# Kernel tuning notes

Measured on AMD Instinct MI355X. Metric: run time of the kernel, lower is better.

The kernel has to match this reference:

```python
import jax, jax.numpy as jnp
import numpy as np

B, C, CI, H, W = 4, 128, 64, 96, 96  # batch, in_channels, inter_channels, spatial
SS = 2                                # sub_sample_factor (maxpool on phi and g)
BN_EPS = 1e-5


def conv1x1(x, w, b):
    # x: [B,C,H,W], w: [O,C], b: [O]
    return jnp.einsum('bchw,oc->bohw', x, w) + b[None, :, None, None]


def maxpool2(x):
    # 2x2 max pool, stride 2. x: [B,C,H,W]
    b, c, h, w = x.shape
    return x.reshape(b, c, h // 2, 2, w // 2, 2).max(axis=(3, 5))


def setup_inputs() -> dict:
    key = jax.random.key(0)
    ks = jax.random.split(key, 12)
    s_in = 1.0 / np.sqrt(C)
    s_ci = 1.0 / np.sqrt(CI)
    return {
        'x':        jax.random.normal(ks[0], (B, C, H, W), jnp.float32),
        'g_w':      jax.random.normal(ks[1], (CI, C), jnp.float32) * s_in,
        'g_b':      jax.random.normal(ks[2], (CI,), jnp.float32) * 0.01,
        'theta_w':  jax.random.normal(ks[3], (CI, C), jnp.float32) * s_in,
        'theta_b':  jax.random.normal(ks[4], (CI,), jnp.float32) * 0.01,
        'phi_w':    jax.random.normal(ks[5], (CI, C), jnp.float32) * s_in,
        'phi_b':    jax.random.normal(ks[6], (CI,), jnp.float32) * 0.01,
        'W_w':      jax.random.normal(ks[7], (C, CI), jnp.float32) * s_ci,
        'W_b':      jax.random.normal(ks[8], (C,), jnp.float32) * 0.01,
        'bn_gamma': jax.random.normal(ks[9], (C,), jnp.float32) * 0.1 + 1.0,
        'bn_beta':  jax.random.normal(ks[10], (C,), jnp.float32) * 0.1,
        'bn_mean':  jax.random.normal(ks[11], (C,), jnp.float32) * 0.1,
        'bn_var':   jax.random.uniform(jax.random.fold_in(key, 99), (C,), jnp.float32, 0.5, 1.5),
    }


def reference(x, g_w, g_b, theta_w, theta_b, phi_w, phi_b, W_w, W_b,
              bn_gamma, bn_beta, bn_mean, bn_var):
    b = x.shape[0]
    # g: conv1x1 -> maxpool(2) -> [B, N_kv, CI]
    g_x = maxpool2(conv1x1(x, g_w, g_b)).reshape(b, CI, -1).transpose(0, 2, 1)
    # theta: conv1x1 -> [B, N_q, CI]
    theta_x = conv1x1(x, theta_w, theta_b).reshape(b, CI, -1).transpose(0, 2, 1)
    # phi: conv1x1 -> maxpool(2) -> [B, CI, N_kv]
    phi_x = maxpool2(conv1x1(x, phi_w, phi_b)).reshape(b, CI, -1)
    # full affinity [B, N_q, N_kv], softmax over keys (embedded_gaussian)
    f = jnp.einsum('bqc,bck->bqk', theta_x, phi_x)
    attn = jax.nn.softmax(f, axis=-1)
    y = jnp.einsum('bqk,bkc->bqc', attn, g_x)            # [B, N_q, CI]
    y = y.transpose(0, 2, 1).reshape(b, CI, H, W)
    # W: conv1x1 (CI -> C) + BatchNorm (inference form) + residual
    W_y = conv1x1(y, W_w, W_b)
    inv = bn_gamma * jax.lax.rsqrt(bn_var + BN_EPS)
    W_y = W_y * inv[None, :, None, None] + (bn_beta - bn_mean * inv)[None, :, None, None]
    return W_y + x
```

## Files before the change

### kernel.cpp

```cpp
#include <hip/hip_runtime.h>
#include <hip/hip_bf16.h>

#define NB 4
#define NC 128
#define NH 96
#define NQ 9216
#define NKV 2304

typedef __bf16 bf8 __attribute__((ext_vector_type(8)));
typedef float f4 __attribute__((ext_vector_type(4)));
typedef unsigned short u16t;
typedef unsigned int u32t;
typedef u32t u32x2 __attribute__((ext_vector_type(2)));

static __device__ __forceinline__ u16t f2bf(float f){
  u32t u = __builtin_bit_cast(u32t, f);
  u = (u + 0x7fffu + ((u >> 16) & 1u)) >> 16;
  return (u16t)u;
}

static __device__ __forceinline__ f4 mfma16(bf8 a, bf8 b, f4 c){
  return __builtin_amdgcn_mfma_f32_16x16x32_bf16(a, b, c, 0, 0, 0);
}

#define GLDS16(gp, lp) __builtin_amdgcn_global_load_lds( \
    (const u32t*)(gp), (u32t*)(lp), 16, 0, 0)

__global__ __launch_bounds__(256) void prep_weights(
    const float* __restrict__ g_w, const float* __restrict__ theta_w,
    const float* __restrict__ phi_w, const float* __restrict__ W_w,
    const float* __restrict__ W_b, const float* __restrict__ bn_gamma,
    const float* __restrict__ bn_beta, const float* __restrict__ bn_mean,
    const float* __restrict__ bn_var,
    u16t* __restrict__ wt_theta, u16t* __restrict__ wt_phi,
    u16t* __restrict__ wt_g, u16t* __restrict__ wt_W,
    float* __restrict__ alpha, float* __restrict__ beta2)
{
  int i = blockIdx.x * 256 + threadIdx.x;
  wt_theta[i] = f2bf(theta_w[i]);
  wt_phi[i]   = f2bf(phi_w[i]);
  wt_g[i]     = f2bf(g_w[i]);
  wt_W[i]     = f2bf(W_w[i]);
  if (blockIdx.x == 0 && threadIdx.x < 128){
    int t = threadIdx.x;
    float inv = bn_gamma[t] * rsqrtf(bn_var[t] + 1e-5f);
    alpha[t] = inv;
    beta2[t] = W_b[t]*inv + bn_beta[t] - bn_mean[t]*inv;
  }
}

__global__ __launch_bounds__(256) void conv3_pool(
    const float* __restrict__ x,
    const u16t* __restrict__ wt_theta, const u16t* __restrict__ wt_phi,
    const u16t* __restrict__ wt_g,
    const float* __restrict__ theta_b, const float* __restrict__ phi_b,
    const float* __restrict__ g_b,
    u16t* __restrict__ theta, u16t* __restrict__ phi, u16t* __restrict__ g_t)
{
  __shared__ __align__(16) u16t xt[64][136];
  const int blk = blockIdx.x;
  const int batch = blk / 144;
  const int t144 = blk % 144;
  const int ph = t144 / 3;
  const int pw0 = (t144 % 3) * 16;
  const int t = threadIdx.x;
  const float* xb = x + (size_t)batch * NC * NQ;

  #pragma unroll
  for (int i = 0; i < 32; ++i){
    int idx = i*256 + t;
    int c = idx >> 6;
    int pl = idx & 63;
    int q = (ph*2 + (pl>>5))*NH + pw0*2 + (pl & 31);
    xt[pl][c] = f2bf(xb[(size_t)c*NQ + q]);
  }
  __syncthreads();

  const int w = t >> 6, l = t & 63, lm = l & 15, lg = l >> 4;
  auto PL = [](int pxi){
    return (((pxi>>1)&1) << 5) + 8*(pxi>>4) + 2*((pxi>>2)&3) + (pxi&1);
  };
  auto QROW = [&](int pxi){
    return (ph*2 + ((pxi>>1)&1))*NH + (pw0 + 4*(pxi>>4) + ((pxi>>2)&3))*2 + (pxi&1);
  };
  bf8 a[4];
  #pragma unroll
  for (int k = 0; k < 4; ++k)
    a[k] = *(const bf8*)&xt[PL(w*16 + lm)][k*32 + lg*8];

  const int kv = ph*48 + pw0 + 4*w + lg;

  f4 Dth[4];
  #pragma unroll
  for (int s = 0; s < 4; ++s){
    float bv = theta_b[s*16 + lm];
    f4 D = {bv, bv, bv, bv};
    #pragma unroll
    for (int k = 0; k < 4; ++k){
      bf8 b = *(const bf8*)&wt_theta[(s*16 + lm)*128 + k*32 + lg*8];
      D = mfma16(a[k], b, D);
    }
    Dth[s] = D;
  }
  {
    u16t* pp = phi + (size_t)batch * NKV * 64;
    #pragma unroll
    for (int s = 0; s < 4; ++s){
      float bv = phi_b[s*16 + lm];
      f4 D = {bv, bv, bv, bv};
      #pragma unroll
      for (int k = 0; k < 4; ++k){
        bf8 b = *(const bf8*)&wt_phi[(s*16 + lm)*128 + k*32 + lg*8];
        D = mfma16(a[k], b, D);
      }
      float mx = fmaxf(fmaxf(D[0], D[1]), fmaxf(D[2], D[3]));
      pp[(size_t)kv*64 + s*16 + lm] = f2bf(mx);
    }
  }
  {
    u16t* gt = g_t + (size_t)batch * 64 * NKV;
    #pragma unroll
    for (int s = 0; s < 4; ++s){
      float bv = g_b[s*16 + lm];
      f4 D = {bv, bv, bv, bv};
      #pragma unroll
      for (int k = 0; k < 4; ++k){
        bf8 b = *(const bf8*)&wt_g[(s*16 + lm)*128 + k*32 + lg*8];
        D = mfma16(a[k], b, D);
      }
      float mx = fmaxf(fmaxf(D[0], D[1]), fmaxf(D[2], D[3]));
      gt[(size_t)(s*16 + lm)*NKV + kv] = f2bf(mx);
    }
  }

  __syncthreads();
  u16t* tl = &xt[0][0];
  #pragma unroll
  for (int s = 0; s < 4; ++s)
    #pragma unroll
    for (int r = 0; r < 4; ++r)
      tl[(w*16 + lg*4 + r)*72 + s*16 + lm] = f2bf(Dth[s][r]);
  __syncthreads();
  {
    u16t* th = theta + (size_t)batch * NQ * 64;
    #pragma unroll
    for (int p = 0; p < 2; ++p){
      int slot = t + 256*p;
      int row = slot >> 3, piece = slot & 7;
      int q = QROW(row);
      *(bf8*)&th[(size_t)q*64 + piece*8] = *(const bf8*)&tl[row*72 + piece*8];
    }
  }
}

__global__ __launch_bounds__(384) void attn_fused(
    const u16t* __restrict__ theta, const u16t* __restrict__ phi,
    const u16t* __restrict__ g_t, const u16t* __restrict__ wt_W,
    const float* __restrict__ alpha, const float* __restrict__ beta2,
    const float* __restrict__ x, float* __restrict__ out)
{
  __shared__ __align__(16) char SM[107008];
  __shared__ float sums[2][144];

  const int bid = blockIdx.x;
  const int blk = (bid & 7)*32 + (bid >> 3);
  const int batch = blk >> 6;
  const int qb = (blk & 63) * 144;
  const int t = threadIdx.x;
  const int w = t >> 6, l = t & 63, lm = l & 15, lg = l >> 4;
  const int qw = w >> 1, kh = w & 1;

  const u16t* th = theta + ((size_t)batch*NQ + qb)*64;
  bf8 a[3][2];
  #pragma unroll
  for (int mr = 0; mr < 3; ++mr){
    a[mr][0] = *(const bf8*)&th[(qw*48 + mr*16 + lm)*64 + lg*8];
    a[mr][1] = *(const bf8*)&th[(qw*48 + mr*16 + lm)*64 + 32 + lg*8];
  }

  const char* phc = (const char*)(phi + (size_t)batch*NKV*64);
  const char* gtc = (const char*)(g_t + (size_t)batch*64*NKV);

  auto STAGE = [&](int kt_s, int buf){
    #pragma unroll
    for (int j = 0; j < 6; ++j){
      int u = w + 6*j;
      if (u < 32){
        int khu = u >> 4, isg = (u >> 3) & 1, sub = u & 7;
        int row = sub*8 + (l >> 3);
        int swz = ((l & 7) ^ (l >> 3)) << 4;
        int kb = (khu*18 + kt_s) * 64;
        char* dst = SM + (isg ? 32768 : 0) + (khu*2 + buf)*8192 + sub*1024 + l*16;
        const char* src = isg
          ? gtc + (size_t)row*(NKV*2) + (size_t)kb*2 + swz
          : phc + (size_t)(kb + row)*128 + swz;
        GLDS16(src, dst);
      }
    }
  };

  f4 Y[3][4];
  #pragma unroll
  for (int mr = 0; mr < 3; ++mr)
    #pragma unroll
    for (int s = 0; s < 4; ++s)
      Y[mr][s] = f4{0.f, 0.f, 0.f, 0.f};
  float lsum[3] = {0.f, 0.f, 0.f};

  u16t* Prow = (u16t*)(SM + 65536 + w*6912);

  STAGE(0, 0);
  asm volatile("s_waitcnt vmcnt(0)" ::: "memory");
  __syncthreads();

  #pragma unroll 2
  for (int kt = 0; kt < 18; ++kt){
    const int buf = kt & 1;
    if (kt + 1 < 18) STAGE(kt + 1, buf ^ 1);
    const char* pb = SM + (kh*2 + buf)*8192;
    const char* gb = SM + 32768 + (kh*2 + buf)*8192;

    bf8 bp[4][2];
    #pragma unroll
    for (int tt = 0; tt < 4; ++tt){
      int rb = (tt*16 + lm)*128;
      int m7 = lm & 7;
      bp[tt][0] = *(const bf8*)(pb + rb + ((lg ^ m7) << 4));
      bp[tt][1] = *(const bf8*)(pb + rb + (((4 + lg) ^ m7) << 4));
    }
    bf8 bg[4][2];
    #pragma unroll
    for (int s = 0; s < 4; ++s){
      int rb = (s*16 + lm)*128;
      int m7 = lm & 7;
      bg[s][0] = *(const bf8*)(gb + rb + ((lg ^ m7) << 4));
      bg[s][1] = *(const bf8*)(gb + rb + (((4 + lg) ^ m7) << 4));
    }
    f4 S[3][4];
    #pragma unroll
    for (int tt = 0; tt < 4; ++tt)
      #pragma unroll
      for (int mr = 0; mr < 3; ++mr){
        f4 z = {0.f, 0.f, 0.f, 0.f};
        z = mfma16(bp[tt][0], a[mr][0], z);
        S[mr][tt] = mfma16(bp[tt][1], a[mr][1], z);
      }
    #pragma unroll
    for (int mr = 0; mr < 3; ++mr)
      #pragma unroll
      for (int tt = 0; tt < 4; ++tt){
        float p0, p1, p2, p3;
        float a0 = fmaf(S[mr][tt][0], 1.44269504f, -43.2808512f);
        float a1 = fmaf(S[mr][tt][1], 1.44269504f, -43.2808512f);
        float a2 = fmaf(S[mr][tt][2], 1.44269504f, -43.2808512f);
        float a3 = fmaf(S[mr][tt][3], 1.44269504f, -43.2808512f);
        asm("v_exp_f32 %0, %1" : "=v"(p0) : "v"(a0));
        asm("v_exp_f32 %0, %1" : "=v"(p1) : "v"(a1));
        asm("v_exp_f32 %0, %1" : "=v"(p2) : "v"(a2));
        asm("v_exp_f32 %0, %1" : "=v"(p3) : "v"(a3));
        lsum[mr] += (p0 + p1) + (p2 + p3);
        u32t lo, hi;
        asm("v_cvt_pk_bf16_f32 %0, %1, %2" : "=v"(lo) : "v"(p0), "v"(p1));
        asm("v_cvt_pk_bf16_f32 %0, %1, %2" : "=v"(hi) : "v"(p2), "v"(p3));
        *(u32x2*)&Prow[(mr*16 + lm)*72 + tt*16 + lg*4] = u32x2{lo, hi};
      }
    #pragma unroll
    for (int mr = 0; mr < 3; ++mr){
      bf8 pa0 = *(const bf8*)&Prow[(mr*16 + lm)*72 + lg*8];
      bf8 pa1 = *(const bf8*)&Prow[(mr*16 + lm)*72 + 32 + lg*8];
      #pragma unroll
      for (int s = 0; s < 4; ++s){
        Y[mr][s] = mfma16(pa0, bg[s][0], Y[mr][s]);
        Y[mr][s] = mfma16(pa1, bg[s][1], Y[mr][s]);
      }
    }
    asm volatile("s_waitcnt vmcnt(0)" ::: "memory");
    __syncthreads();
  }

  #pragma unroll
  for (int mr = 0; mr < 3; ++mr){
    float sv = lsum[mr];
    sv += __shfl_xor(sv, 16);
    sv += __shfl_xor(sv, 32);
    if (lg == 0) sums[kh][qw*48 + mr*16 + lm] = sv;
  }

  float (*yp)[68] = (float (*)[68])SM;
  if (kh == 0){
    #pragma unroll
    for (int mr = 0; mr < 3; ++mr)
      #pragma unroll
      for (int s = 0; s < 4; ++s)
        #pragma unroll
        for (int r = 0; r < 4; ++r)
          yp[qw*48 + mr*16 + lg*4 + r][s*16 + lm] = Y[mr][s][r];
  }
  __syncthreads();
  if (kh == 1){
    #pragma unroll
    for (int mr = 0; mr < 3; ++mr)
      #pragma unroll
      for (int s = 0; s < 4; ++s)
        #pragma unroll
        for (int r = 0; r < 4; ++r)
          yp[qw*48 + mr*16 + lg*4 + r][s*16 + lm] += Y[mr][s][r];
  }
  __syncthreads();

  u16t* yl = (u16t*)(SM + 75264);
  #pragma unroll
  for (int i = 0; i < 12; ++i){
    int p = t + 384*i;
    int q = p >> 5, cp = p & 31;
    float tot = sums[0][q] + sums[1][q];
    float inv = 1.0f / tot;
    float v0 = yp[q][cp*2] * inv;
    float v1 = yp[q][cp*2 + 1] * inv;
    u32t pk;
    asm("v_cvt_pk_bf16_f32 %0, %1, %2" : "=v"(pk) : "v"(v0), "v"(v1));
    *(u32t*)&yl[q*72 + cp*2] = pk;
  }
  __syncthreads();

  float (*ol)[130] = (float (*)[130])SM;
  #pragma unroll
  for (int i = 0; i < 12; ++i){
    int tau = w + 6*i;
    int qt = tau >> 3, ct = tau & 7;
    bf8 ya0 = *(const bf8*)&yl[(qt*16 + lm)*72 + lg*8];
    bf8 ya1 = *(const bf8*)&yl[(qt*16 + lm)*72 + 32 + lg*8];
    const u16t* wr = wt_W + (ct*16 + lm)*64;
    bf8 b0 = *(const bf8*)&wr[lg*8];
    bf8 b1 = *(const bf8*)&wr[lg*8 + 32];
    f4 z = {0.f, 0.f, 0.f, 0.f};
    z = mfma16(ya0, b0, z);
    z = mfma16(ya1, b1, z);
    #pragma unroll
    for (int r = 0; r < 4; ++r)
      ol[qt*16 + lg*4 + r][ct*16 + lm] = z[r];
  }
  __syncthreads();

  const float* xb = x + (size_t)batch*NC*NQ + qb;
  float* ob = out + (size_t)batch*NC*NQ + qb;
  #pragma unroll
  for (int i = 0; i < 12; ++i){
    int idx = t + 384*i;
    int c = idx / 36, qv = idx % 36;
    float4 xv = *(const float4*)&xb[(size_t)c*NQ + qv*4];
    float al = alpha[c], be = beta2[c];
    float4 ov;
    ov.x = ol[qv*4 + 0][c]*al + be + xv.x;
    ov.y = ol[qv*4 + 1][c]*al + be + xv.y;
    ov.z = ol[qv*4 + 2][c]*al + be + xv.z;
    ov.w = ol[qv*4 + 3][c]*al + be + xv.w;
    *(float4*)&ob[(size_t)c*NQ + qv*4] = ov;
  }
}

extern "C" void kernel_launch(void* const* d_in, const int* in_sizes, int n_in,
                              void* d_out, int out_size, void* d_ws, size_t ws_size,
                              hipStream_t stream)
{
  const float* x       = (const float*)d_in[0];
  const float* g_w     = (const float*)d_in[1];
  const float* g_b     = (const float*)d_in[2];
  const float* theta_w = (const float*)d_in[3];
  const float* theta_b = (const float*)d_in[4];
  const float* phi_w   = (const float*)d_in[5];
  const float* phi_b   = (const float*)d_in[6];
  const float* W_w     = (const float*)d_in[7];
  const float* W_b     = (const float*)d_in[8];
  const float* bn_g    = (const float*)d_in[9];
  const float* bn_b    = (const float*)d_in[10];
  const float* bn_m    = (const float*)d_in[11];
  const float* bn_v    = (const float*)d_in[12];
  float* out = (float*)d_out;

  char* ws = (char*)d_ws;
  size_t off = 0;
  u16t* theta = (u16t*)(ws + off); off += (size_t)NB*NQ*64*2;
  u16t* phi   = (u16t*)(ws + off); off += (size_t)NB*NKV*64*2;
  u16t* g_t   = (u16t*)(ws + off); off += (size_t)NB*64*NKV*2;
  u16t* wt_theta = (u16t*)(ws + off); off += 64*128*2;
  u16t* wt_phi   = (u16t*)(ws + off); off += 64*128*2;
  u16t* wt_g     = (u16t*)(ws + off); off += 64*128*2;
  u16t* wt_W     = (u16t*)(ws + off); off += 128*64*2;
  float* alpha = (float*)(ws + off); off += 128*4;
  float* beta2 = (float*)(ws + off); off += 128*4;
  if (off > ws_size) return;

  prep_weights<<<32, 256, 0, stream>>>(g_w, theta_w, phi_w, W_w, W_b,
                                       bn_g, bn_b, bn_m, bn_v,
                                       wt_theta, wt_phi, wt_g, wt_W, alpha, beta2);
  conv3_pool<<<576, 256, 0, stream>>>(x, wt_theta, wt_phi, wt_g,
                                      theta_b, phi_b, g_b, theta, phi, g_t);
  attn_fused<<<256, 384, 0, stream>>>(theta, phi, g_t, wt_W, alpha, beta2, x, out);
}
```

Before: 86.53 us.

## Triple-buffer K/V staging with counted waits, setprio around MFMA, float4 x loads

The attention kernel moves from double to triple buffering of the phi and g tiles. It prefetches two tiles ahead and uses vmcnt-counted waits with raw barriers instead of a full drain each iteration. Every wave now issues exactly six async loads per stage, with the extras going to a scratch LDS area, so the vmcnt counts stay uniform. MFMA sections are wrapped in s_setprio, and the conv kernel loads x as float4. The larger LDS footprint (about 140KB) and the scratch loads use extra bandwidth and may limit occupancy.

Result: faster. 81.02 us (-6.4%).

```diff
diff --git a/kernel.cpp b/kernel.cpp
--- a/kernel.cpp
+++ b/kernel.cpp
@@ -67,12 +67,18 @@
   const float* xb = x + (size_t)batch * NC * NQ;
 
   #pragma unroll
-  for (int i = 0; i < 32; ++i){
-    int idx = i*256 + t;
-    int c = idx >> 6;
-    int pl = idx & 63;
-    int q = (ph*2 + (pl>>5))*NH + pw0*2 + (pl & 31);
-    xt[pl][c] = f2bf(xb[(size_t)c*NQ + q]);
+  for (int i = 0; i < 8; ++i){
+    int slot = i*256 + t;
+    int c = slot >> 4;
+    int quad = slot & 15;
+    int row = quad >> 3, col4 = (quad & 7)*4;
+    int q = (ph*2 + row)*NH + pw0*2 + col4;
+    float4 v = *(const float4*)&xb[(size_t)c*NQ + q];
+    int pl = row*32 + col4;
+    xt[pl+0][c] = f2bf(v.x);
+    xt[pl+1][c] = f2bf(v.y);
+    xt[pl+2][c] = f2bf(v.z);
+    xt[pl+3][c] = f2bf(v.w);
   }
   __syncthreads();
 
@@ -153,13 +159,18 @@
   }
 }
 
+#define PHI_OFF 0
+#define G_OFF   49152
+#define P_OFF   98304
+#define SCRAP_OFF 139776
+
 __global__ __launch_bounds__(384) void attn_fused(
     const u16t* __restrict__ theta, const u16t* __restrict__ phi,
     const u16t* __restrict__ g_t, const u16t* __restrict__ wt_W,
     const float* __restrict__ alpha, const float* __restrict__ beta2,
     const float* __restrict__ x, float* __restrict__ out)
 {
-  __shared__ __align__(16) char SM[107008];
+  __shared__ __align__(16) char SM[143872];
   __shared__ float sums[2][144];
 
   const int bid = blockIdx.x;
@@ -177,25 +188,27 @@
     a[mr][0] = *(const bf8*)&th[(qw*48 + mr*16 + lm)*64 + lg*8];
     a[mr][1] = *(const bf8*)&th[(qw*48 + mr*16 + lm)*64 + 32 + lg*8];
   }
+  asm volatile("s_waitcnt vmcnt(0)" ::: "memory");
 
   const char* phc = (const char*)(phi + (size_t)batch*NKV*64);
   const char* gtc = (const char*)(g_t + (size_t)batch*64*NKV);
 
-  auto STAGE = [&](int kt_s, int buf){
+  auto STAGE = [&](int kt_s, int bufc){
     #pragma unroll
     for (int j = 0; j < 6; ++j){
-      int u = w + 6*j;
-      if (u < 32){
-        int khu = u >> 4, isg = (u >> 3) & 1, sub = u & 7;
-        int row = sub*8 + (l >> 3);
-        int swz = ((l & 7) ^ (l >> 3)) << 4;
-        int kb = (khu*18 + kt_s) * 64;
-        char* dst = SM + (isg ? 32768 : 0) + (khu*2 + buf)*8192 + sub*1024 + l*16;
-        const char* src = isg
-          ? gtc + (size_t)row*(NKV*2) + (size_t)kb*2 + swz
-          : phc + (size_t)(kb + row)*128 + swz;
-        GLDS16(src, dst);
-      }
+      int u = w*6 + j;
+      int ur = (u < 32) ? u : (u - 32);
+      int khu = ur >> 4, isg = (ur >> 3) & 1, sub = ur & 7;
+      int row = sub*8 + (l >> 3);
+      int swz = ((l & 7) ^ (l >> 3)) << 4;
+      int kb = (khu*18 + kt_s) * 64;
+      char* dst = (u < 32)
+        ? SM + (isg ? G_OFF : PHI_OFF) + (khu*3 + bufc)*8192 + sub*1024 + l*16
+        : SM + SCRAP_OFF + (u - 32)*1024 + l*16;
+      const char* src = isg
+        ? gtc + (size_t)row*(NKV*2) + (size_t)kb*2 + swz
+        : phc + (size_t)(kb + row)*128 + swz;
+      GLDS16(src, dst);
     }
   };
 
@@ -207,18 +220,26 @@
       Y[mr][s] = f4{0.f, 0.f, 0.f, 0.f};
   float lsum[3] = {0.f, 0.f, 0.f};
 
-  u16t* Prow = (u16t*)(SM + 65536 + w*6912);
+  u16t* Prow = (u16t*)(SM + P_OFF + w*6912);
 
   STAGE(0, 0);
-  asm volatile("s_waitcnt vmcnt(0)" ::: "memory");
-  __syncthreads();
-
-  #pragma unroll 2
+  STAGE(1, 1);
+
+  int bufc = 0;
   for (int kt = 0; kt < 18; ++kt){
-    const int buf = kt & 1;
-    if (kt + 1 < 18) STAGE(kt + 1, buf ^ 1);
-    const char* pb = SM + (kh*2 + buf)*8192;
-    const char* gb = SM + 32768 + (kh*2 + buf)*8192;
+    __builtin_amdgcn_s_barrier();
+    if (kt < 16){
+      STAGE(kt + 2, (bufc == 0) ? 2 : bufc - 1);
+      asm volatile("s_waitcnt vmcnt(12)" ::: "memory");
+    } else if (kt == 16){
+      asm volatile("s_waitcnt vmcnt(6)" ::: "memory");
+    } else {
+      asm volatile("s_waitcnt vmcnt(0)" ::: "memory");
+    }
+    __builtin_amdgcn_s_barrier();
+
+    const char* pb = SM + PHI_OFF + (kh*3 + bufc)*8192;
+    const char* gb = SM + G_OFF   + (kh*3 + bufc)*8192;
 
     bf8 bp[4][2];
     #pragma unroll
@@ -237,6 +258,7 @@
       bg[s][1] = *(const bf8*)(gb + rb + (((4 + lg) ^ m7) << 4));
     }
     f4 S[3][4];
+    __builtin_amdgcn_s_setprio(1);
     #pragma unroll
     for (int tt = 0; tt < 4; ++tt)
       #pragma unroll
@@ -245,6 +267,7 @@
         z = mfma16(bp[tt][0], a[mr][0], z);
         S[mr][tt] = mfma16(bp[tt][1], a[mr][1], z);
       }
+    __builtin_amdgcn_s_setprio(0);
     #pragma unroll
     for (int mr = 0; mr < 3; ++mr)
       #pragma unroll
@@ -264,6 +287,7 @@
         asm("v_cvt_pk_bf16_f32 %0, %1, %2" : "=v"(hi) : "v"(p2), "v"(p3));
         *(u32x2*)&Prow[(mr*16 + lm)*72 + tt*16 + lg*4] = u32x2{lo, hi};
       }
+    __builtin_amdgcn_s_setprio(1);
     #pragma unroll
     for (int mr = 0; mr < 3; ++mr){
       bf8 pa0 = *(const bf8*)&Prow[(mr*16 + lm)*72 + lg*8];
@@ -274,8 +298,8 @@
         Y[mr][s] = mfma16(pa1, bg[s][1], Y[mr][s]);
       }
     }
-    asm volatile("s_waitcnt vmcnt(0)" ::: "memory");
-    __syncthreads();
+    __builtin_amdgcn_s_setprio(0);
+    bufc = (bufc == 2) ? 0 : bufc + 1;
   }
 
   #pragma unroll
@@ -286,6 +310,7 @@
     if (lg == 0) sums[kh][qw*48 + mr*16 + lm] = sv;
   }
 
+  __syncthreads();
   float (*yp)[68] = (float (*)[68])SM;
   if (kh == 0){
     #pragma unroll
@@ -308,7 +333,7 @@
   }
   __syncthreads();
 
-  u16t* yl = (u16t*)(SM + 75264);
+  u16t* yl = (u16t*)(SM + P_OFF);
   #pragma unroll
   for (int i = 0; i < 12; ++i){
     int p = t + 384*i;
```
